# Optimization experiments

Measured on AMD Instinct MI355X. Metric: run time of the kernel, lower is better.

The kernel has to match this reference:

```python
import jax, jax.numpy as jnp
import numpy as np

N_NODES = 50000
N_EDGES = 800000
DIM = 100

def setup_inputs() -> dict:
    key = jax.random.key(0)
    k1, k2, k3, k4, k5, k6 = jax.random.split(key, 6)
    ego_embedding = jax.random.normal(k1, (N_NODES, DIM), dtype=jnp.float32)
    edge_src = jax.random.randint(k2, (N_EDGES,), 0, N_NODES, dtype=jnp.int32)
    edge_dst = jax.random.randint(k3, (N_EDGES,), 0, N_NODES, dtype=jnp.int32)
    edge_weight = jax.random.uniform(k4, (N_EDGES,), dtype=jnp.float32)
    W = jax.random.normal(k5, (DIM, DIM), dtype=jnp.float32) * (1.0 / np.sqrt(DIM))
    b = jax.random.normal(k6, (DIM,), dtype=jnp.float32) * 0.01
    return {"ego_embedding": ego_embedding, "edge_src": edge_src,
            "edge_dst": edge_dst, "edge_weight": edge_weight, "W": W, "b": b}

def reference(ego_embedding, edge_src, edge_dst, edge_weight, W, b):
    # Linear projection: h = x @ W^T + b  (torch Linear convention)
    hidden = ego_embedding @ W.T + b                    # [N, D]
    # u_mul_e: message on each edge = h[src] * edge_weight
    msgs = hidden[edge_src] * edge_weight[:, None]       # [E, D]
    # sum reduce into destination nodes
    out = jax.ops.segment_sum(msgs, edge_dst, num_segments=N_NODES)  # [N, D]
    return out
```

## Files before the change

### kernel.cpp

```cpp
#include <hip/hip_runtime.h>

#define N_NODES 50000
#define N_EDGES 800000
#define DIM 100

#define NB      1563
#define CAPB    768
#define OVF_CAP 4096
#define EPB     8192
#define BIN_BLOCKS  98
#define GEMM_BLOCKS 625
#define ROWS_PB 80

#define HIDB_OFF  0u
#define GCUR_OFF  10000000u
#define OVFC_OFF  10006256u
#define OVF_OFF   10006272u
#define BKT2_OFF  10071808u
#define WT_OFF    19674880u
#define WS_NEED   19714880u

__device__ inline unsigned bf16hi(float v) {
    unsigned u = __float_as_uint(v);
    u += 0x7FFFu + ((u >> 16) & 1u);
    return u & 0xFFFF0000u;
}
__device__ inline unsigned bf16pair(float lo, float hi) {
    unsigned ulo = __float_as_uint(lo); ulo += 0x7FFFu + ((ulo >> 16) & 1u);
    unsigned uhi = __float_as_uint(hi); uhi += 0x7FFFu + ((uhi >> 16) & 1u);
    return (ulo >> 16) | (uhi & 0xFFFF0000u);
}

__global__ __launch_bounds__(256) void srgnn_transpose(
    const float* __restrict__ W, float* __restrict__ Wt,
    int* __restrict__ gcur, int* __restrict__ ovfc)
{
    const unsigned i = blockIdx.x * 256u + threadIdx.x;
    if (i < DIM * DIM) {
        const int c = i / DIM, k = i - c * DIM;
        Wt[k * DIM + c] = W[i];
    }
    if (i < NB) gcur[i] = 0;
    if (i == 0) *ovfc = 0;
}

__global__ __launch_bounds__(512) void srgnn_gemm_bin(
    const float* __restrict__ x, const float* __restrict__ Wtg,
    const float* __restrict__ b, unsigned* __restrict__ hidU,
    const int* __restrict__ esrc, const int* __restrict__ edst,
    const float* __restrict__ ew, int* __restrict__ gcur,
    int* __restrict__ ovfc, int4* __restrict__ ovf, uint2* __restrict__ bkt2)
{
    __shared__ __align__(16) char smem[72000];
    const int t = threadIdx.x;

    if (blockIdx.x < BIN_BLOCKS) {
        int* hist = (int*)smem;
        int* lcur = hist + NB;
        const int e0 = blockIdx.x * EPB;

        for (int i = t; i < NB; i += 512) hist[i] = 0;
        __syncthreads();

        int d[16];
        #pragma unroll
        for (int k = 0; k < 16; ++k) {
            const int e = e0 + t + k * 512;
            d[k] = (e < N_EDGES) ? edst[e] : -1;
            if (d[k] >= 0) atomicAdd(&hist[d[k] >> 5], 1);
        }
        __syncthreads();
        for (int i = t; i < NB; i += 512)
            if (hist[i]) lcur[i] = atomicAdd(&gcur[i], hist[i]);
        __syncthreads();
        #pragma unroll
        for (int k = 0; k < 16; ++k) {
            if (d[k] >= 0) {
                const int e = e0 + t + k * 512;
                const int s = esrc[e];
                const float w = ew[e];
                const int bq = d[k] >> 5;
                const int pos = atomicAdd(&lcur[bq], 1);
                if (pos < CAPB) {
                    bkt2[(size_t)bq * CAPB + pos] =
                        make_uint2((unsigned)s | bf16hi(w), (unsigned)d[k]);
                } else {
                    const int op = atomicAdd(ovfc, 1);
                    if (op < OVF_CAP) ovf[op] = make_int4(d[k], s, __float_as_int(w), 0);
                }
            }
        }
    } else {
        float (*Wt)[DIM] = (float (*)[DIM])smem;
        float (*xs)[DIM] = (float (*)[DIM])(smem + 40000);
        const int row0 = (blockIdx.x - BIN_BLOCKS) * ROWS_PB;

        for (int i = t; i < 2500; i += 512) {
            const float4 v = *reinterpret_cast<const float4*>(&Wtg[i * 4]);
            *reinterpret_cast<float4*>(&Wt[0][0] + i * 4) = v;
        }
        for (int i = t; i < ROWS_PB * 25; i += 512) {
            const int r = i / 25, c4 = (i - r * 25) * 4;
            const float4 v = *reinterpret_cast<const float4*>(
                &x[(size_t)(row0 + r) * DIM + c4]);
            *reinterpret_cast<float4*>(&xs[r][c4]) = v;
        }
        __syncthreads();

        if (t < 500) {
            const int g  = t / 25;
            const int c4 = (t - g * 25) * 4;
            const float4 bv = *reinterpret_cast<const float4*>(&b[c4]);
            float4 a0 = bv, a1 = bv, a2 = bv, a3 = bv;

            #pragma unroll 4
            for (int k = 0; k < DIM; ++k) {
                const float4 wv = *reinterpret_cast<const float4*>(&Wt[k][c4]);
                const float x0 = xs[g     ][k];
                const float x1 = xs[g + 20][k];
                const float x2 = xs[g + 40][k];
                const float x3 = xs[g + 60][k];
                a0.x += x0 * wv.x; a0.y += x0 * wv.y; a0.z += x0 * wv.z; a0.w += x0 * wv.w;
                a1.x += x1 * wv.x; a1.y += x1 * wv.y; a1.z += x1 * wv.z; a1.w += x1 * wv.w;
                a2.x += x2 * wv.x; a2.y += x2 * wv.y; a2.z += x2 * wv.z; a2.w += x2 * wv.w;
                a3.x += x3 * wv.x; a3.y += x3 * wv.y; a3.z += x3 * wv.z; a3.w += x3 * wv.w;
            }
            const int u0 = c4 >> 1;
            uint2 p;
            p.x = bf16pair(a0.x, a0.y); p.y = bf16pair(a0.z, a0.w);
            *reinterpret_cast<uint2*>(&hidU[(size_t)(row0 + g     ) * 50 + u0]) = p;
            p.x = bf16pair(a1.x, a1.y); p.y = bf16pair(a1.z, a1.w);
            *reinterpret_cast<uint2*>(&hidU[(size_t)(row0 + g + 20) * 50 + u0]) = p;
            p.x = bf16pair(a2.x, a2.y); p.y = bf16pair(a2.z, a2.w);
            *reinterpret_cast<uint2*>(&hidU[(size_t)(row0 + g + 40) * 50 + u0]) = p;
            p.x = bf16pair(a3.x, a3.y); p.y = bf16pair(a3.z, a3.w);
            *reinterpret_cast<uint2*>(&hidU[(size_t)(row0 + g + 60) * 50 + u0]) = p;
        }
    }
}

__global__ __launch_bounds__(256) void srgnn_agg_s32(
    const unsigned* __restrict__ hidU, const int* __restrict__ gcur,
    const uint2* __restrict__ bkt2, const int* __restrict__ ovfc,
    const int4* __restrict__ ovf, float* __restrict__ out)
{
    __shared__ uint2    recs[CAPB];
    __shared__ unsigned srt[CAPB];
    __shared__ int nh[32], sc[32], cur[32];

    const int t = threadIdx.x;
    const int bq = blockIdx.x;
    int cntb = gcur[bq];
    if (cntb > CAPB) cntb = CAPB;

    if (t < 32) nh[t] = 0;
    __syncthreads();
    for (int i = t; i < cntb; i += 256) {
        const uint2 r = bkt2[(size_t)bq * CAPB + i];
        recs[i] = r;
        atomicAdd(&nh[r.y & 31], 1);
    }
    __syncthreads();
    if (t < 32) sc[t] = nh[t];
    __syncthreads();
    for (int ofs = 1; ofs < 32; ofs <<= 1) {
        int a = 0;
        if (t < 32 && t >= ofs) a = sc[t - ofs];
        __syncthreads();
        if (t < 32) sc[t] += a;
        __syncthreads();
    }
    if (t < 32) cur[t] = sc[t] - nh[t];
    __syncthreads();
    for (int i = t; i < cntb; i += 256) {
        const uint2 r = recs[i];
        const int pos = atomicAdd(&cur[r.y & 31], 1);
        srt[pos] = r.x;
    }
    __syncthreads();

    int oc = *ovfc;
    if (oc > OVF_CAP) oc = OVF_CAP;
    const int lane = t & 63;
    const int wid  = t >> 6;
    const bool active = (lane < 50);

    for (int q = 0; q < 8; ++q) {
        const int n  = wid * 8 + q;
        const int s1 = sc[n];
        const int s0 = s1 - nh[n];
        float2 acc = make_float2(0.f, 0.f);

        int p = s0;
        for (; p + 8 <= s1; p += 8) {
            unsigned r[8], h[8];
            #pragma unroll
            for (int j = 0; j < 8; ++j) r[j] = srt[p + j];
            if (active) {
                #pragma unroll
                for (int j = 0; j < 8; ++j)
                    h[j] = hidU[(size_t)(r[j] & 0xFFFFu) * 50 + lane];
                #pragma unroll
                for (int j = 0; j < 8; ++j) {
                    const float wj = __uint_as_float(r[j] & 0xFFFF0000u);
                    acc.x += wj * __uint_as_float(h[j] << 16);
                    acc.y += wj * __uint_as_float(h[j] & 0xFFFF0000u);
                }
            }
        }
        for (; p < s1; ++p) {
            const unsigned r = srt[p];
            const float wi = __uint_as_float(r & 0xFFFF0000u);
            if (active) {
                const unsigned h = hidU[(size_t)(r & 0xFFFFu) * 50 + lane];
                acc.x += wi * __uint_as_float(h << 16);
                acc.y += wi * __uint_as_float(h & 0xFFFF0000u);
            }
        }

        const int ng = bq * 32 + n;
        if (oc > 0) {
            for (int i = 0; i < oc; ++i) {
                const int4 v = ovf[i];
                if (v.x == ng && active) {
                    const unsigned h = hidU[(size_t)v.y * 50 + lane];
                    const float wi = __int_as_float(v.z);
                    acc.x += wi * __uint_as_float(h << 16);
                    acc.y += wi * __uint_as_float(h & 0xFFFF0000u);
                }
            }
        }
        if (ng < N_NODES && active)
            *reinterpret_cast<float2*>(&out[(size_t)ng * DIM + 2 * lane]) = acc;
    }
}

__global__ __launch_bounds__(256) void srgnn_gemm_bias(
    const float* __restrict__ x, const float* __restrict__ W,
    const float* __restrict__ b, float* __restrict__ hidden)
{
    __shared__ float Wt[DIM][DIM + 4];
    __shared__ float bs[DIM];
    __shared__ float xs[8][DIM];
    const int t = threadIdx.x;
    for (int i = t; i < DIM * DIM; i += 256) {
        int c = i / DIM, k = i - c * DIM;
        Wt[k][c] = W[i];
    }
    if (t < DIM) bs[t] = b[t];
    const int row0 = blockIdx.x * 8;
    for (int i = t; i < 8 * DIM; i += 256) {
        int r = i / DIM, k = i - r * DIM;
        int row = row0 + r;
        xs[r][k] = (row < N_NODES) ? x[row * DIM + k] : 0.0f;
    }
    __syncthreads();
    if (t < 200) {
        const int r  = t / 25;
        const int c4 = (t - r * 25) * 4;
        float acc0 = bs[c4 + 0], acc1 = bs[c4 + 1], acc2 = bs[c4 + 2], acc3 = bs[c4 + 3];
        for (int k = 0; k < DIM; ++k) {
            const float xv = xs[r][k];
            const float4 wv = *reinterpret_cast<const float4*>(&Wt[k][c4]);
            acc0 += xv * wv.x; acc1 += xv * wv.y; acc2 += xv * wv.z; acc3 += xv * wv.w;
        }
        const int row = row0 + r;
        if (row < N_NODES)
            *reinterpret_cast<float4*>(&hidden[row * DIM + c4]) =
                make_float4(acc0, acc1, acc2, acc3);
    }
}

__global__ __launch_bounds__(256) void srgnn_scatter_atomic(
    const float* __restrict__ hidden, const int* __restrict__ esrc,
    const int* __restrict__ edst, const float* __restrict__ ew,
    float* __restrict__ out)
{
    const unsigned gid = blockIdx.x * 256u + threadIdx.x;
    const unsigned e = gid / 25u;
    const unsigned j = gid - e * 25u;
    if (e >= N_EDGES) return;
    const int   s  = esrc[e];
    const int   d  = edst[e];
    const float wt = ew[e];
    const float4 h = *reinterpret_cast<const float4*>(&hidden[(size_t)s * DIM + j * 4]);
    float* op = &out[(size_t)d * DIM + j * 4];
    atomicAdd(op + 0, h.x * wt);
    atomicAdd(op + 1, h.y * wt);
    atomicAdd(op + 2, h.z * wt);
    atomicAdd(op + 3, h.w * wt);
}

extern "C" void kernel_launch(void* const* d_in, const int* in_sizes, int n_in,
                              void* d_out, int out_size, void* d_ws, size_t ws_size,
                              hipStream_t stream) {
    const float* x    = (const float*)d_in[0];
    const int*   esrc = (const int*)  d_in[1];
    const int*   edst = (const int*)  d_in[2];
    const float* ew   = (const float*)d_in[3];
    const float* W    = (const float*)d_in[4];
    const float* b    = (const float*)d_in[5];
    float* out = (float*)d_out;

    char* ws = (char*)d_ws;

    if (ws_size >= WS_NEED) {
        unsigned* hidU = (unsigned*)(ws + HIDB_OFF);
        int*      gcur = (int*)     (ws + GCUR_OFF);
        int*      ovfc = (int*)     (ws + OVFC_OFF);
        int4*     ovf  = (int4*)    (ws + OVF_OFF);
        uint2*    bkt2 = (uint2*)   (ws + BKT2_OFF);
        float*    Wt   = (float*)   (ws + WT_OFF);

        srgnn_transpose<<<(DIM * DIM + 255) / 256, 256, 0, stream>>>(W, Wt, gcur, ovfc);
        srgnn_gemm_bin<<<BIN_BLOCKS + GEMM_BLOCKS, 512, 0, stream>>>(
            x, Wt, b, hidU, esrc, edst, ew, gcur, ovfc, ovf, bkt2);
        srgnn_agg_s32<<<NB, 256, 0, stream>>>(hidU, gcur, bkt2, ovfc, ovf, out);
    } else {
        float* hidden = (float*)ws;
        hipMemsetAsync(d_out, 0, (size_t)out_size * sizeof(float), stream);
        const int gemm_blocks = (N_NODES + 7) / 8;
        srgnn_gemm_bias<<<gemm_blocks, 256, 0, stream>>>(x, W, b, hidden);
        const long long work = (long long)N_EDGES * 25;
        const int scat_blocks = (int)((work + 255) / 256);
        srgnn_scatter_atomic<<<scat_blocks, 256, 0, stream>>>(hidden, esrc, edst, ew, out);
    }
}
```

Before: 72.26 us.

## Aggregate raw inputs first, then apply linear projection per destination

Reorders the computation as segment_sum(x[src]*w) @ W^T + (sum of w)*b. The dense GEMM on all nodes before gathering is removed, and the projection now runs inside the aggregation kernel on 32 node rows per block using a bf16 W held in LDS. The first kernel now bins edges, packs x to bf16 and packs W, with smaller bin blocks. The transpose kernel is replaced by a memset. The GEMM now happens after aggregation, so each aggregation block does extra LDS-bound compute, and W is also rounded to bf16, which lowers precision.

```diff
diff --git a/kernel.cpp b/kernel.cpp
--- a/kernel.cpp
+++ b/kernel.cpp
@@ -4,21 +4,21 @@
 #define N_EDGES 800000
 #define DIM 100
 
-#define NB      1563
-#define CAPB    768
-#define OVF_CAP 4096
-#define EPB     8192
-#define BIN_BLOCKS  98
-#define GEMM_BLOCKS 625
-#define ROWS_PB 80
-
-#define HIDB_OFF  0u
+#define NB       1563
+#define CAPB     768
+#define OVF_CAP  4096
+#define EPB      4096
+#define BIN_BLOCKS  196
+#define PACK_BLOCKS 306
+#define XB_UINTS 2500000
+
+#define XB_OFF    0u
 #define GCUR_OFF  10000000u
-#define OVFC_OFF  10006256u
-#define OVF_OFF   10006272u
-#define BKT2_OFF  10071808u
-#define WT_OFF    19674880u
-#define WS_NEED   19714880u
+#define OVFC_OFF  10006272u
+#define OVF_OFF   10006288u
+#define BKT_OFF   10071824u
+#define WTU_OFF   19674896u
+#define WS_NEED   19694896u
 
 __device__ inline unsigned bf16hi(float v) {
     unsigned u = __float_as_uint(v);
@@ -31,40 +31,26 @@
     return (ulo >> 16) | (uhi & 0xFFFF0000u);
 }
 
-__global__ __launch_bounds__(256) void srgnn_transpose(
-    const float* __restrict__ W, float* __restrict__ Wt,
-    int* __restrict__ gcur, int* __restrict__ ovfc)
+__global__ __launch_bounds__(512) void srgnn_prep_bin(
+    const float* __restrict__ x, const float* __restrict__ W,
+    const int* __restrict__ esrc, const int* __restrict__ edst,
+    const float* __restrict__ ew, unsigned* __restrict__ xb,
+    unsigned* __restrict__ WtU, int* __restrict__ gcur,
+    int* __restrict__ ovfc, int4* __restrict__ ovf, uint2* __restrict__ bkt)
 {
-    const unsigned i = blockIdx.x * 256u + threadIdx.x;
-    if (i < DIM * DIM) {
-        const int c = i / DIM, k = i - c * DIM;
-        Wt[k * DIM + c] = W[i];
-    }
-    if (i < NB) gcur[i] = 0;
-    if (i == 0) *ovfc = 0;
-}
-
-__global__ __launch_bounds__(512) void srgnn_gemm_bin(
-    const float* __restrict__ x, const float* __restrict__ Wtg,
-    const float* __restrict__ b, unsigned* __restrict__ hidU,
-    const int* __restrict__ esrc, const int* __restrict__ edst,
-    const float* __restrict__ ew, int* __restrict__ gcur,
-    int* __restrict__ ovfc, int4* __restrict__ ovf, uint2* __restrict__ bkt2)
-{
-    __shared__ __align__(16) char smem[72000];
+    __shared__ int hist[NB];
+    __shared__ int lcur[NB];
     const int t = threadIdx.x;
 
     if (blockIdx.x < BIN_BLOCKS) {
-        int* hist = (int*)smem;
-        int* lcur = hist + NB;
         const int e0 = blockIdx.x * EPB;
 
         for (int i = t; i < NB; i += 512) hist[i] = 0;
         __syncthreads();
 
-        int d[16];
+        int d[8];
         #pragma unroll
-        for (int k = 0; k < 16; ++k) {
+        for (int k = 0; k < 8; ++k) {
             const int e = e0 + t + k * 512;
             d[k] = (e < N_EDGES) ? edst[e] : -1;
             if (d[k] >= 0) atomicAdd(&hist[d[k] >> 5], 1);
@@ -74,7 +60,7 @@
             if (hist[i]) lcur[i] = atomicAdd(&gcur[i], hist[i]);
         __syncthreads();
         #pragma unroll
-        for (int k = 0; k < 16; ++k) {
+        for (int k = 0; k < 8; ++k) {
             if (d[k] >= 0) {
                 const int e = e0 + t + k * 512;
                 const int s = esrc[e];
@@ -82,7 +68,7 @@
                 const int bq = d[k] >> 5;
                 const int pos = atomicAdd(&lcur[bq], 1);
                 if (pos < CAPB) {
-                    bkt2[(size_t)bq * CAPB + pos] =
+                    bkt[(size_t)bq * CAPB + pos] =
                         make_uint2((unsigned)s | bf16hi(w), (unsigned)d[k]);
                 } else {
                     const int op = atomicAdd(ovfc, 1);
@@ -90,73 +76,53 @@
                 }
             }
         }
+    } else if (blockIdx.x < BIN_BLOCKS + PACK_BLOCKS) {
+        const int pb = blockIdx.x - BIN_BLOCKS;
+        #pragma unroll
+        for (int k = 0; k < 16; ++k) {
+            const unsigned i = (unsigned)pb * 8192u + t + k * 512u;
+            if (i < XB_UINTS) {
+                const float2 v = *reinterpret_cast<const float2*>(&x[2 * (size_t)i]);
+                xb[i] = bf16pair(v.x, v.y);
+            }
+        }
     } else {
-        float (*Wt)[DIM] = (float (*)[DIM])smem;
-        float (*xs)[DIM] = (float (*)[DIM])(smem + 40000);
-        const int row0 = (blockIdx.x - BIN_BLOCKS) * ROWS_PB;
-
-        for (int i = t; i < 2500; i += 512) {
-            const float4 v = *reinterpret_cast<const float4*>(&Wtg[i * 4]);
-            *reinterpret_cast<float4*>(&Wt[0][0] + i * 4) = v;
-        }
-        for (int i = t; i < ROWS_PB * 25; i += 512) {
-            const int r = i / 25, c4 = (i - r * 25) * 4;
-            const float4 v = *reinterpret_cast<const float4*>(
-                &x[(size_t)(row0 + r) * DIM + c4]);
-            *reinterpret_cast<float4*>(&xs[r][c4]) = v;
-        }
-        __syncthreads();
-
-        if (t < 500) {
-            const int g  = t / 25;
-            const int c4 = (t - g * 25) * 4;
-            const float4 bv = *reinterpret_cast<const float4*>(&b[c4]);
-            float4 a0 = bv, a1 = bv, a2 = bv, a3 = bv;
-
-            #pragma unroll 4
-            for (int k = 0; k < DIM; ++k) {
-                const float4 wv = *reinterpret_cast<const float4*>(&Wt[k][c4]);
-                const float x0 = xs[g     ][k];
-                const float x1 = xs[g + 20][k];
-                const float x2 = xs[g + 40][k];
-                const float x3 = xs[g + 60][k];
-                a0.x += x0 * wv.x; a0.y += x0 * wv.y; a0.z += x0 * wv.z; a0.w += x0 * wv.w;
-                a1.x += x1 * wv.x; a1.y += x1 * wv.y; a1.z += x1 * wv.z; a1.w += x1 * wv.w;
-                a2.x += x2 * wv.x; a2.y += x2 * wv.y; a2.z += x2 * wv.z; a2.w += x2 * wv.w;
-                a3.x += x3 * wv.x; a3.y += x3 * wv.y; a3.z += x3 * wv.z; a3.w += x3 * wv.w;
-            }
-            const int u0 = c4 >> 1;
-            uint2 p;
-            p.x = bf16pair(a0.x, a0.y); p.y = bf16pair(a0.z, a0.w);
-            *reinterpret_cast<uint2*>(&hidU[(size_t)(row0 + g     ) * 50 + u0]) = p;
-            p.x = bf16pair(a1.x, a1.y); p.y = bf16pair(a1.z, a1.w);
-            *reinterpret_cast<uint2*>(&hidU[(size_t)(row0 + g + 20) * 50 + u0]) = p;
-            p.x = bf16pair(a2.x, a2.y); p.y = bf16pair(a2.z, a2.w);
-            *reinterpret_cast<uint2*>(&hidU[(size_t)(row0 + g + 40) * 50 + u0]) = p;
-            p.x = bf16pair(a3.x, a3.y); p.y = bf16pair(a3.z, a3.w);
-            *reinterpret_cast<uint2*>(&hidU[(size_t)(row0 + g + 60) * 50 + u0]) = p;
-        }
-    }
-}
-
-__global__ __launch_bounds__(256) void srgnn_agg_s32(
-    const unsigned* __restrict__ hidU, const int* __restrict__ gcur,
-    const uint2* __restrict__ bkt2, const int* __restrict__ ovfc,
-    const int4* __restrict__ ovf, float* __restrict__ out)
+        for (int i = t; i < DIM * 50; i += 512) {
+            const int k = i / 50, c2 = i - k * 50;
+            WtU[i] = bf16pair(W[(2 * c2) * DIM + k], W[(2 * c2 + 1) * DIM + k]);
+        }
+    }
+}
+
+__global__ __launch_bounds__(256) void srgnn_agg_gemm(
+    const unsigned* __restrict__ xb, const int* __restrict__ gcur,
+    const uint2* __restrict__ bkt, const int* __restrict__ ovfc,
+    const int4* __restrict__ ovf, const unsigned* __restrict__ WtUg,
+    const float* __restrict__ b, float* __restrict__ out)
 {
-    __shared__ uint2    recs[CAPB];
+    __shared__ __align__(16) unsigned WtLDS[DIM * 50];
+    __shared__ __align__(16) char ubuf[12800];
     __shared__ unsigned srt[CAPB];
     __shared__ int nh[32], sc[32], cur[32];
+    __shared__ float sums[32];
+
+    uint2* recs = reinterpret_cast<uint2*>(ubuf);
+    float (*rows)[DIM] = reinterpret_cast<float (*)[DIM]>(ubuf);
 
     const int t = threadIdx.x;
     const int bq = blockIdx.x;
-    int cntb = gcur[bq];
-    if (cntb > CAPB) cntb = CAPB;
+
+    for (int i = t; i < 1250; i += 256)
+        reinterpret_cast<uint4*>(WtLDS)[i] =
+            reinterpret_cast<const uint4*>(WtUg)[i];
+
+    const int craw = gcur[bq];
+    const int cntb = (craw > CAPB) ? CAPB : craw;
 
     if (t < 32) nh[t] = 0;
     __syncthreads();
     for (int i = t; i < cntb; i += 256) {
-        const uint2 r = bkt2[(size_t)bq * CAPB + i];
+        const uint2 r = bkt[(size_t)bq * CAPB + i];
         recs[i] = r;
         atomicAdd(&nh[r.y & 31], 1);
     }
@@ -190,16 +156,20 @@
         const int s1 = sc[n];
         const int s0 = s1 - nh[n];
         float2 acc = make_float2(0.f, 0.f);
+        float sumw = 0.f;
 
         int p = s0;
         for (; p + 8 <= s1; p += 8) {
             unsigned r[8], h[8];
             #pragma unroll
             for (int j = 0; j < 8; ++j) r[j] = srt[p + j];
+            #pragma unroll
+            for (int j = 0; j < 8; ++j)
+                sumw += __uint_as_float(r[j] & 0xFFFF0000u);
             if (active) {
                 #pragma unroll
                 for (int j = 0; j < 8; ++j)
-                    h[j] = hidU[(size_t)(r[j] & 0xFFFFu) * 50 + lane];
+                    h[j] = xb[(size_t)(r[j] & 0xFFFFu) * 50 + lane];
                 #pragma unroll
                 for (int j = 0; j < 8; ++j) {
                     const float wj = __uint_as_float(r[j] & 0xFFFF0000u);
@@ -211,27 +181,58 @@
         for (; p < s1; ++p) {
             const unsigned r = srt[p];
             const float wi = __uint_as_float(r & 0xFFFF0000u);
+            sumw += wi;
             if (active) {
-                const unsigned h = hidU[(size_t)(r & 0xFFFFu) * 50 + lane];
+                const unsigned h = xb[(size_t)(r & 0xFFFFu) * 50 + lane];
                 acc.x += wi * __uint_as_float(h << 16);
                 acc.y += wi * __uint_as_float(h & 0xFFFF0000u);
             }
         }
 
         const int ng = bq * 32 + n;
-        if (oc > 0) {
+        if (craw > CAPB && oc > 0) {
             for (int i = 0; i < oc; ++i) {
                 const int4 v = ovf[i];
-                if (v.x == ng && active) {
-                    const unsigned h = hidU[(size_t)v.y * 50 + lane];
+                if (v.x == ng) {
                     const float wi = __int_as_float(v.z);
-                    acc.x += wi * __uint_as_float(h << 16);
-                    acc.y += wi * __uint_as_float(h & 0xFFFF0000u);
+                    sumw += wi;
+                    if (active) {
+                        const unsigned h = xb[(size_t)v.y * 50 + lane];
+                        acc.x += wi * __uint_as_float(h << 16);
+                        acc.y += wi * __uint_as_float(h & 0xFFFF0000u);
+                    }
                 }
             }
         }
-        if (ng < N_NODES && active)
-            *reinterpret_cast<float2*>(&out[(size_t)ng * DIM + 2 * lane]) = acc;
+        if (active) {
+            rows[n][2 * lane]     = acc.x;
+            rows[n][2 * lane + 1] = acc.y;
+        }
+        if (lane == 0) sums[n] = sumw;
+    }
+    __syncthreads();
+
+    {
+        const int n = t >> 3;
+        const int q = t & 7;
+        const int ng = bq * 32 + n;
+        if (ng < N_NODES) {
+            const float sw = sums[n];
+            for (int c2 = q; c2 < 50; c2 += 8) {
+                const float2 bv = *reinterpret_cast<const float2*>(&b[2 * c2]);
+                float ax = sw * bv.x;
+                float ay = sw * bv.y;
+                #pragma unroll 4
+                for (int k = 0; k < DIM; ++k) {
+                    const float rk = rows[n][k];
+                    const unsigned u = WtLDS[k * 50 + c2];
+                    ax += rk * __uint_as_float(u << 16);
+                    ay += rk * __uint_as_float(u & 0xFFFF0000u);
+                }
+                *reinterpret_cast<float2*>(&out[(size_t)ng * DIM + 2 * c2]) =
+                    make_float2(ax, ay);
+            }
+        }
     }
 }
 
@@ -305,17 +306,18 @@
     char* ws = (char*)d_ws;
 
     if (ws_size >= WS_NEED) {
-        unsigned* hidU = (unsigned*)(ws + HIDB_OFF);
+        unsigned* xb   = (unsigned*)(ws + XB_OFF);
         int*      gcur = (int*)     (ws + GCUR_OFF);
         int*      ovfc = (int*)     (ws + OVFC_OFF);
         int4*     ovf  = (int4*)    (ws + OVF_OFF);
-        uint2*    bkt2 = (uint2*)   (ws + BKT2_OFF);
-        float*    Wt   = (float*)   (ws + WT_OFF);
-
-        srgnn_transpose<<<(DIM * DIM + 255) / 256, 256, 0, stream>>>(W, Wt, gcur, ovfc);
-        srgnn_gemm_bin<<<BIN_BLOCKS + GEMM_BLOCKS, 512, 0, stream>>>(
-            x, Wt, b, hidU, esrc, edst, ew, gcur, ovfc, ovf, bkt2);
-        srgnn_agg_s32<<<NB, 256, 0, stream>>>(hidU, gcur, bkt2, ovfc, ovf, out);
+        uint2*    bkt  = (uint2*)   (ws + BKT_OFF);
+        unsigned* WtU  = (unsigned*)(ws + WTU_OFF);
+
+        hipMemsetAsync(gcur, 0, (OVFC_OFF - GCUR_OFF) + 16, stream);
+        srgnn_prep_bin<<<BIN_BLOCKS + PACK_BLOCKS + 1, 512, 0, stream>>>(
+            x, W, esrc, edst, ew, xb, WtU, gcur, ovfc, ovf, bkt);
+        srgnn_agg_gemm<<<NB, 256, 0, stream>>>(
+            xb, gcur, bkt, ovfc, ovf, WtU, b, out);
     } else {
         float* hidden = (float*)ws;
         hipMemsetAsync(d_out, 0, (size_t)out_size * sizeof(float), stream);
```

Result: slower. 110.2 us (+52.5%).
